# Optimization experiments

Hardware: AMD Instinct MI355X
Metric: run time of the kernel (lower is better)

## Reference

```python
import jax, jax.numpy as jnp
import numpy as np

N_NODES = 50000
N_EDGES = 500000
FEAT = 64
HEADS = 4


def setup_inputs() -> dict:
    key = jax.random.key(0)
    ks = jax.random.split(key, 8)
    x = jax.random.normal(ks[0], (N_NODES, FEAT), jnp.float32)
    edge_index = jax.random.randint(ks[1], (2, N_EDGES), 0, N_NODES)
    edge_vec = jax.random.normal(ks[2], (N_EDGES, 3), jnp.float32)
    edge_len = jax.random.uniform(ks[3], (N_EDGES,), jnp.float32)
    # learned parameters
    w_proj = jax.random.normal(ks[4], (HEADS, FEAT, FEAT), jnp.float32) / np.float32(np.sqrt(FEAT))
    xav = np.float32(np.sqrt(6.0 / (HEADS + FEAT)))
    radial_score = jax.random.uniform(ks[5], (HEADS, FEAT), jnp.float32, -xav, xav)
    tangential_score = jax.random.uniform(ks[6], (HEADS, FEAT), jnp.float32, -xav, xav)
    radial_distance_scale = jnp.array(1.0, jnp.float32)
    w_out = jax.random.normal(ks[7], (FEAT, FEAT), jnp.float32) / np.float32(np.sqrt(FEAT))
    return {
        "x": x,
        "edge_index": edge_index,
        "edge_vec": edge_vec,
        "edge_len": edge_len,
        "w_proj": w_proj,
        "radial_score": radial_score,
        "tangential_score": tangential_score,
        "radial_distance_scale": radial_distance_scale,
        "w_out": w_out,
    }


def reference(x, edge_index, edge_vec, edge_len, w_proj, radial_score,
              tangential_score, radial_distance_scale, w_out):
    # edge_vec is accepted by the original forward but never used.
    sender, receiver = edge_index[0], edge_index[1]
    num_nodes = x.shape[0]
    # per-head projection: [N,H,F]
    proj = jnp.einsum('nf,hfg->nhg', x, w_proj)
    # edge deltas: [E,H,F]
    delta = proj[sender] - proj[receiver]
    # logits: [E,H]
    radial_logits = jnp.einsum('ehf,hf->eh', delta, radial_score) \
        - radial_distance_scale * edge_len[:, None]
    tangential_logits = jnp.einsum('ehf,hf->eh', delta, tangential_score)

    def seg_softmax_msg(logits):
        # segment softmax over edges grouped by receiver (equivalent to the
        m = jax.ops.segment_max(logits, receiver, num_segments=num_nodes)  # [N,H]
        e = jnp.exp(logits - m[receiver])                                  # [E,H]
        s = jax.ops.segment_sum(e, receiver, num_segments=num_nodes)      # [N,H]
        alpha = e / s[receiver]                                            # [E,H]
        # weighted scatter-sum of deltas -> [N,H,F]
        return jax.ops.segment_sum(alpha[:, :, None] * delta, receiver,
                                   num_segments=num_nodes)

    out = (seg_softmax_msg(radial_logits) + seg_softmax_msg(tangential_logits))
    out = out.mean(axis=1)  # mean over heads -> [N,F]
    out = jnp.nan_to_num(out)
    return x + out @ w_out
```

## Files before the change

kernel.cpp:

```cpp
#include <hip/hip_runtime.h>

#define NN 50000
#define NE 500000
#define CAP 40

static __device__ __forceinline__ unsigned short f2b(float f) {
    union { float f; unsigned int u; } v; v.f = f;
    unsigned int u = v.u;
    unsigned int r = (u + 0x7FFFu + ((u >> 16) & 1u)) >> 16;
    return (unsigned short)r;
}
static __device__ __forceinline__ float b2f(unsigned short b) {
    union { unsigned int u; float f; } v; v.u = ((unsigned int)b) << 16;
    return v.f;
}

static __device__ __forceinline__ void finish_node(
    int n, float4 a, float4 r4, float4 t4, int lane, int h, int gq,
    float2* __restrict__ rst, unsigned short* __restrict__ projb)
{
    float pr = a.x * r4.x + a.y * r4.y + a.z * r4.z + a.w * r4.w;
    float pt = a.x * t4.x + a.y * t4.y + a.z * t4.z + a.w * t4.w;
    #pragma unroll
    for (int m = 1; m < 16; m <<= 1) {
        pr += __shfl_xor(pr, m);
        pt += __shfl_xor(pt, m);
    }
    if (gq == 0) rst[n * 4 + h] = make_float2(pr, pt);
    ushort4 pb;
    pb.x = f2b(a.x); pb.y = f2b(a.y); pb.z = f2b(a.z); pb.w = f2b(a.w);
    *((ushort4*)(projb + (size_t)n * 256 + lane * 4)) = pb;
}

__global__ __launch_bounds__(256) void k_proj(
    const float* __restrict__ x, const float* __restrict__ wp,
    const float* __restrict__ rsc, const float* __restrict__ tsc,
    unsigned short* __restrict__ projb, float2* __restrict__ rst,
    int* __restrict__ cnt)
{
    __shared__ float lw[4 * 64 * 64];
    int tid = threadIdx.x;
    int gtid = blockIdx.x * 256 + tid;
    if (gtid < NN) cnt[gtid] = 0;
    for (int i = tid; i < 4096; i += 256)
        ((float4*)lw)[i] = ((const float4*)wp)[i];
    __syncthreads();

    int lane = tid & 63, wid = tid >> 6;
    int h = lane >> 4, gq = lane & 15;
    const float4* wrow = (const float4*)(lw + h * 4096);
    float4 r4 = *(const float4*)(rsc + h * 64 + gq * 4);
    float4 t4 = *(const float4*)(tsc + h * 64 + gq * 4);

    int gw = blockIdx.x * 4 + wid;
    int n0 = gw * 4;
    if (n0 >= NN) return;
    float xv0 = x[(n0 + 0) * 64 + lane];
    float xv1 = x[(n0 + 1) * 64 + lane];
    float xv2 = x[(n0 + 2) * 64 + lane];
    float xv3 = x[(n0 + 3) * 64 + lane];
    float4 a0 = {0,0,0,0}, a1 = {0,0,0,0}, a2 = {0,0,0,0}, a3 = {0,0,0,0};
    #pragma unroll 4
    for (int k = 0; k < 64; ++k) {
        float4 w4 = wrow[k * 16 + gq];
        float k0 = __shfl(xv0, k), k1 = __shfl(xv1, k);
        float k2 = __shfl(xv2, k), k3 = __shfl(xv3, k);
        a0.x += k0 * w4.x; a0.y += k0 * w4.y; a0.z += k0 * w4.z; a0.w += k0 * w4.w;
        a1.x += k1 * w4.x; a1.y += k1 * w4.y; a1.z += k1 * w4.z; a1.w += k1 * w4.w;
        a2.x += k2 * w4.x; a2.y += k2 * w4.y; a2.z += k2 * w4.z; a2.w += k2 * w4.w;
        a3.x += k3 * w4.x; a3.y += k3 * w4.y; a3.z += k3 * w4.z; a3.w += k3 * w4.w;
    }
    finish_node(n0 + 0, a0, r4, t4, lane, h, gq, rst, projb);
    finish_node(n0 + 1, a1, r4, t4, lane, h, gq, rst, projb);
    finish_node(n0 + 2, a2, r4, t4, lane, h, gq, rst, projb);
    finish_node(n0 + 3, a3, r4, t4, lane, h, gq, rst, projb);
}

__global__ __launch_bounds__(256) void k_place(
    const int* __restrict__ ei, const float* __restrict__ elen,
    int* __restrict__ cnt, int2* __restrict__ sedge)
{
    int e = blockIdx.x * 256 + threadIdx.x;
    if (e >= NE) return;
    int s = ei[e], r = ei[NE + e];
    int slot = atomicAdd(&cnt[r], 1);
    if (slot >= CAP) return;
    int2 v;
    v.x = s;
    v.y = __float_as_int(elen[e]);
    sedge[r * CAP + slot] = v;
}

__global__ __launch_bounds__(256, 8) void k_msg(
    const float* __restrict__ x, const unsigned short* __restrict__ projb,
    const int* __restrict__ cnt, const int2* __restrict__ sedge,
    const float2* __restrict__ rst, const float* __restrict__ scale_p,
    const float* __restrict__ wout, float* __restrict__ out)
{
    __shared__ float lwT[64 * 68];
    int tid = threadIdx.x;
    for (int i = tid; i < 4096; i += 256) {
        int f = i >> 6, g = i & 63;
        lwT[g * 68 + f] = wout[i];
    }

    int lane = tid & 63, wid = tid >> 6;
    int h = lane >> 4, q = lane & 15, grp = h << 4;
    int n = blockIdx.x * 4 + wid;

    float outv = x[n * 64 + lane];
    int cn = cnt[n]; if (cn > CAP) cn = CAP;
    float sc = scale_p[0];

    float4 ar = {0.f,0.f,0.f,0.f}, at = {0.f,0.f,0.f,0.f};
    float srl = 0.f, stl = 0.f;

#define ROWLD(SJ) (*(const ushort4*)(projb + ((size_t)(SJ) << 8) + (lane << 2)))
#define CONS(P, IDX) { \
    float cr = __shfl(erq, grp + (IDX)); \
    float ct = __shfl(etq, grp + (IDX)); \
    float p0 = b2f((P).x), p1 = b2f((P).y), p2 = b2f((P).z), p3 = b2f((P).w); \
    ar.x += cr * p0; ar.y += cr * p1; ar.z += cr * p2; ar.w += cr * p3; \
    at.x += ct * p0; at.y += ct * p1; at.z += ct * p2; at.w += ct * p3; }

    if (cn > 0) {
        float2 rr = rst[n * 4 + h];
        int rowb = n * CAP;
        for (int base = 0; base < cn; base += 12) {
            int bc = cn - base; if (bc > 12) bc = 12;
            int2 ed = sedge[rowb + base + q];
            int sq = (q < bc) ? ed.x : n;
            float len = __int_as_float(ed.y);
            float2 srt = rst[sq * 4 + h];
            float erq = __expf(srt.x - rr.x - sc * len);
            float etq = __expf(srt.y - rr.y);
            if (q >= bc) { erq = 0.f; etq = 0.f; }
            srl += erq; stl += etq;
            int s0 = __shfl(sq, 0);
            ushort4 pA = ROWLD(s0);
            ushort4 pB = ROWLD((1  < bc) ? __shfl(sq, 1)  : s0);
            ushort4 pC = ROWLD((2  < bc) ? __shfl(sq, 2)  : s0);
            ushort4 pD = ROWLD((3  < bc) ? __shfl(sq, 3)  : s0);
            ushort4 pE = ROWLD((4  < bc) ? __shfl(sq, 4)  : s0);
            ushort4 pF = ROWLD((5  < bc) ? __shfl(sq, 5)  : s0);
            ushort4 pG = ROWLD((6  < bc) ? __shfl(sq, 6)  : s0);
            ushort4 pH = ROWLD((7  < bc) ? __shfl(sq, 7)  : s0);
            ushort4 pI = ROWLD((8  < bc) ? __shfl(sq, 8)  : s0);
            ushort4 pJ = ROWLD((9  < bc) ? __shfl(sq, 9)  : s0);
            ushort4 pK = ROWLD((10 < bc) ? __shfl(sq, 10) : s0);
            ushort4 pL = ROWLD((11 < bc) ? __shfl(sq, 11) : s0);
            CONS(pA, 0)  CONS(pB, 1)  CONS(pC, 2)  CONS(pD, 3)
            CONS(pE, 4)  CONS(pF, 5)  CONS(pG, 6)  CONS(pH, 7)
            CONS(pI, 8)  CONS(pJ, 9)  CONS(pK, 10) CONS(pL, 11)
        }
        #pragma unroll
        for (int m = 1; m < 16; m <<= 1) {
            srl += __shfl_xor(srl, m);
            stl += __shfl_xor(stl, m);
        }
        float isr = 1.0f / srl, ist = 1.0f / stl;
        ushort4 pr = ROWLD(n);
        ar.x = isr * ar.x + ist * at.x - 2.f * b2f(pr.x);
        ar.y = isr * ar.y + ist * at.y - 2.f * b2f(pr.y);
        ar.z = isr * ar.z + ist * at.z - 2.f * b2f(pr.z);
        ar.w = isr * ar.w + ist * at.w - 2.f * b2f(pr.w);
    }
    ar.x += __shfl_xor(ar.x, 16); ar.y += __shfl_xor(ar.y, 16);
    ar.z += __shfl_xor(ar.z, 16); ar.w += __shfl_xor(ar.w, 16);
    ar.x += __shfl_xor(ar.x, 32); ar.y += __shfl_xor(ar.y, 32);
    ar.z += __shfl_xor(ar.z, 32); ar.w += __shfl_xor(ar.w, 32);
    float4 m4 = make_float4(0.25f * ar.x, 0.25f * ar.y, 0.25f * ar.z, 0.25f * ar.w);

    __syncthreads();

    const float* wTg = lwT + lane * 68;
    #pragma unroll
    for (int j = 0; j < 16; ++j) {
        float4 wv = *(const float4*)(wTg + j * 4);
        outv += __shfl(m4.x, j) * wv.x + __shfl(m4.y, j) * wv.y
              + __shfl(m4.z, j) * wv.z + __shfl(m4.w, j) * wv.w;
    }
    out[n * 64 + lane] = outv;
#undef ROWLD
#undef CONS
}

extern "C" void kernel_launch(void* const* d_in, const int* in_sizes, int n_in,
                              void* d_out, int out_size, void* d_ws, size_t ws_size,
                              hipStream_t stream) {
    const float* x       = (const float*)d_in[0];
    const int*   ei      = (const int*)d_in[1];
    const float* elen    = (const float*)d_in[3];
    const float* wp      = (const float*)d_in[4];
    const float* rsc     = (const float*)d_in[5];
    const float* tsc     = (const float*)d_in[6];
    const float* scale_p = (const float*)d_in[7];
    const float* wout    = (const float*)d_in[8];
    float* out = (float*)d_out;

    char* ws = (char*)d_ws;
    size_t off = 0;
    auto alloc = [&](size_t bytes) {
        void* p = ws + off;
        off = (off + bytes + 255) & ~(size_t)255;
        return p;
    };
    unsigned short* projb = (unsigned short*)alloc((size_t)NN * 256 * 2);
    float2* rst   = (float2*)alloc((size_t)NN * 4 * 8);
    int*    cnt   = (int*)alloc((size_t)NN * 4);
    int2*   sedge = (int2*)alloc(((size_t)NN * CAP + 64) * 8);

    k_proj<<<3125, 256, 0, stream>>>(x, wp, rsc, tsc, projb, rst, cnt);
    k_place<<<(NE + 255) / 256, 256, 0, stream>>>(ei, elen, cnt, sedge);
    k_msg<<<12500, 256, 0, stream>>>(x, projb, cnt, sedge, rst, scale_p, wout, out);
}
```

Before: 270.6 us.

## Precompute per-edge softmax exponentials in bucketing kernel as packed bf16

Moves the exp of the radial and tangential logits for every edge and head out of the message kernel and into the edge-bucketing kernel. The results are stored as packed bf16 pairs next to a separate sender index array. This removes the random rst gathers and exp work from the latency-bound message loop. In exchange the bucketing kernel does more gathers and writes 16 extra bytes per edge, and the exps lose precision from bf16 rounding. Masked lanes now also load row n unconditionally instead of s0.

```diff
diff --git a/kernel.cpp b/kernel.cpp
--- a/kernel.cpp
+++ b/kernel.cpp
@@ -13,6 +13,9 @@
 static __device__ __forceinline__ float b2f(unsigned short b) {
     union { unsigned int u; float f; } v; v.u = ((unsigned int)b) << 16;
     return v.f;
+}
+static __device__ __forceinline__ unsigned int pack2(float a, float b) {
+    return (unsigned int)f2b(a) | ((unsigned int)f2b(b) << 16);
 }
 
 static __device__ __forceinline__ void finish_node(
@@ -76,25 +79,36 @@
     finish_node(n0 + 3, a3, r4, t4, lane, h, gq, rst, projb);
 }
 
-__global__ __launch_bounds__(256) void k_place(
+__global__ __launch_bounds__(256) void k_bucket(
     const int* __restrict__ ei, const float* __restrict__ elen,
-    int* __restrict__ cnt, int2* __restrict__ sedge)
+    const float* __restrict__ rst_f,
+    const float* __restrict__ scale_p,
+    int* __restrict__ cnt, int* __restrict__ ssend, uint4* __restrict__ scrh)
 {
     int e = blockIdx.x * 256 + threadIdx.x;
     if (e >= NE) return;
     int s = ei[e], r = ei[NE + e];
+    float d = scale_p[0] * elen[e];
+    float4 ss0 = *(const float4*)(rst_f + s * 8);
+    float4 ss1 = *(const float4*)(rst_f + s * 8 + 4);
+    float4 rr0 = *(const float4*)(rst_f + r * 8);
+    float4 rr1 = *(const float4*)(rst_f + r * 8 + 4);
     int slot = atomicAdd(&cnt[r], 1);
     if (slot >= CAP) return;
-    int2 v;
-    v.x = s;
-    v.y = __float_as_int(elen[e]);
-    sedge[r * CAP + slot] = v;
+    int idx = r * CAP + slot;
+    ssend[idx] = s;
+    uint4 rec;
+    rec.x = pack2(__expf(ss0.x - rr0.x - d), __expf(ss0.y - rr0.y));
+    rec.y = pack2(__expf(ss0.z - rr0.z - d), __expf(ss0.w - rr0.w));
+    rec.z = pack2(__expf(ss1.x - rr1.x - d), __expf(ss1.y - rr1.y));
+    rec.w = pack2(__expf(ss1.z - rr1.z - d), __expf(ss1.w - rr1.w));
+    scrh[idx] = rec;
 }
 
 __global__ __launch_bounds__(256, 8) void k_msg(
     const float* __restrict__ x, const unsigned short* __restrict__ projb,
-    const int* __restrict__ cnt, const int2* __restrict__ sedge,
-    const float2* __restrict__ rst, const float* __restrict__ scale_p,
+    const int* __restrict__ cnt, const int* __restrict__ ssend,
+    const unsigned int* __restrict__ scrh_u,
     const float* __restrict__ wout, float* __restrict__ out)
 {
     __shared__ float lwT[64 * 68];
@@ -110,7 +124,6 @@
 
     float outv = x[n * 64 + lane];
     int cn = cnt[n]; if (cn > CAP) cn = CAP;
-    float sc = scale_p[0];
 
     float4 ar = {0.f,0.f,0.f,0.f}, at = {0.f,0.f,0.f,0.f};
     float srl = 0.f, stl = 0.f;
@@ -124,31 +137,30 @@
     at.x += ct * p0; at.y += ct * p1; at.z += ct * p2; at.w += ct * p3; }
 
     if (cn > 0) {
-        float2 rr = rst[n * 4 + h];
         int rowb = n * CAP;
         for (int base = 0; base < cn; base += 12) {
             int bc = cn - base; if (bc > 12) bc = 12;
-            int2 ed = sedge[rowb + base + q];
-            int sq = (q < bc) ? ed.x : n;
-            float len = __int_as_float(ed.y);
-            float2 srt = rst[sq * 4 + h];
-            float erq = __expf(srt.x - rr.x - sc * len);
-            float etq = __expf(srt.y - rr.y);
-            if (q >= bc) { erq = 0.f; etq = 0.f; }
+            int sv = ssend[rowb + base + q];
+            unsigned cw = scrh_u[(size_t)(rowb + base + q) * 4 + h];
+            int sq = (q < bc) ? sv : n;
+            float erq = 0.f, etq = 0.f;
+            if (q < bc) {
+                erq = b2f((unsigned short)(cw & 0xffff));
+                etq = b2f((unsigned short)(cw >> 16));
+            }
             srl += erq; stl += etq;
-            int s0 = __shfl(sq, 0);
-            ushort4 pA = ROWLD(s0);
-            ushort4 pB = ROWLD((1  < bc) ? __shfl(sq, 1)  : s0);
-            ushort4 pC = ROWLD((2  < bc) ? __shfl(sq, 2)  : s0);
-            ushort4 pD = ROWLD((3  < bc) ? __shfl(sq, 3)  : s0);
-            ushort4 pE = ROWLD((4  < bc) ? __shfl(sq, 4)  : s0);
-            ushort4 pF = ROWLD((5  < bc) ? __shfl(sq, 5)  : s0);
-            ushort4 pG = ROWLD((6  < bc) ? __shfl(sq, 6)  : s0);
-            ushort4 pH = ROWLD((7  < bc) ? __shfl(sq, 7)  : s0);
-            ushort4 pI = ROWLD((8  < bc) ? __shfl(sq, 8)  : s0);
-            ushort4 pJ = ROWLD((9  < bc) ? __shfl(sq, 9)  : s0);
-            ushort4 pK = ROWLD((10 < bc) ? __shfl(sq, 10) : s0);
-            ushort4 pL = ROWLD((11 < bc) ? __shfl(sq, 11) : s0);
+            ushort4 pA = ROWLD(__shfl(sq, 0));
+            ushort4 pB = ROWLD(__shfl(sq, 1));
+            ushort4 pC = ROWLD(__shfl(sq, 2));
+            ushort4 pD = ROWLD(__shfl(sq, 3));
+            ushort4 pE = ROWLD(__shfl(sq, 4));
+            ushort4 pF = ROWLD(__shfl(sq, 5));
+            ushort4 pG = ROWLD(__shfl(sq, 6));
+            ushort4 pH = ROWLD(__shfl(sq, 7));
+            ushort4 pI = ROWLD(__shfl(sq, 8));
+            ushort4 pJ = ROWLD(__shfl(sq, 9));
+            ushort4 pK = ROWLD(__shfl(sq, 10));
+            ushort4 pL = ROWLD(__shfl(sq, 11));
             CONS(pA, 0)  CONS(pB, 1)  CONS(pC, 2)  CONS(pD, 3)
             CONS(pE, 4)  CONS(pF, 5)  CONS(pG, 6)  CONS(pH, 7)
             CONS(pI, 8)  CONS(pJ, 9)  CONS(pK, 10) CONS(pL, 11)
@@ -208,9 +220,12 @@
     unsigned short* projb = (unsigned short*)alloc((size_t)NN * 256 * 2);
     float2* rst   = (float2*)alloc((size_t)NN * 4 * 8);
     int*    cnt   = (int*)alloc((size_t)NN * 4);
-    int2*   sedge = (int2*)alloc(((size_t)NN * CAP + 64) * 8);
+    int*    ssend = (int*)alloc(((size_t)NN * CAP + 64) * 4);
+    uint4*  scrh  = (uint4*)alloc(((size_t)NN * CAP + 64) * 16);
 
     k_proj<<<3125, 256, 0, stream>>>(x, wp, rsc, tsc, projb, rst, cnt);
-    k_place<<<(NE + 255) / 256, 256, 0, stream>>>(ei, elen, cnt, sedge);
-    k_msg<<<12500, 256, 0, stream>>>(x, projb, cnt, sedge, rst, scale_p, wout, out);
-}
+    k_bucket<<<(NE + 255) / 256, 256, 0, stream>>>(ei, elen, (const float*)rst,
+                                                   scale_p, cnt, ssend, scrh);
+    k_msg<<<12500, 256, 0, stream>>>(x, projb, cnt, ssend,
+                                     (const unsigned int*)scrh, wout, out);
+}
```

Result: no change. 271.7 us (+0.4%).
